# Kernel tuning notes

Measured on AMD Instinct MI355X. Metric: run time of the kernel, lower is better.

The kernel has to match this reference:

```python
import jax, jax.numpy as jnp
import numpy as np

VOCAB = 512
T = 64
D = 32
N_NODES = 4000
N_LAYERS = 5
EDGE_P = 0.03
N_BIAS = 2
SEED = 0
BATCH = 512
N_IN = T * D  # 2048 input nodes (flattened [T, d_model])


def build_graph():
    """Deterministic layered random-wired DAG.

    Node layout: [0, N_IN) inputs | [N_IN, N_IN+N_BIAS) bias(=1) |
    hidden layers | last VOCAB nodes = outputs (logits).
    An edge (u -> v) exists with prob EDGE_P for any u in an earlier
    layer than v; every non-input node gets >=1 incoming edge.
    Returns (layers, total_edges) where each layer entry is
    (src_ids, dst_local, layer_start, layer_size, w_lo, w_hi).
    """
    rng = np.random.RandomState(SEED)
    n_hidden = N_NODES - (N_IN + N_BIAS) - VOCAB
    sizes = [n_hidden // N_LAYERS + (1 if i < n_hidden % N_LAYERS else 0)
             for i in range(N_LAYERS)] + [VOCAB]
    layers = []
    start = N_IN + N_BIAS  # nodes with ids < start are valid sources
    offset = 0
    for size in sizes:
        mask = rng.random((start, size)) < EDGE_P
        empty = np.where(mask.sum(axis=0) == 0)[0]
        if empty.size:
            mask[rng.randint(0, start, empty.size), empty] = True
        src, dst = np.nonzero(mask)
        n_e = src.size
        layers.append((src.astype(np.int32), dst.astype(np.int32),
                       start, size, offset, offset + n_e))
        offset += n_e
        start += size
    return layers, offset


def setup_inputs() -> dict:
    key = jax.random.key(0)
    k1, k2, k3, k4 = jax.random.split(key, 4)
    _, n_edges = build_graph()
    return {
        "ids": jax.random.randint(k1, (BATCH, T), 0, VOCAB),
        "token_emb": jax.random.normal(k2, (VOCAB, D), dtype=jnp.float32) * 0.02,
        "pos_emb": jax.random.normal(k3, (T, D), dtype=jnp.float32) * 0.02,
        "weights": jax.random.normal(k4, (n_edges,), dtype=jnp.float32) * 0.05,
    }


def reference(ids, token_emb, pos_emb, weights):
    layers, _ = build_graph()  # static (numpy, trace-time)
    B = ids.shape[0]
    # embedding lookup + positional add, flatten to the RWNN input slab
    emb = token_emb[ids] + pos_emb[None, :, :]          # [B, T, D]
    flat = emb.reshape(B, N_IN)                          # [B, n_in]
    vals = jnp.concatenate(
        [flat, jnp.ones((B, N_BIAS), flat.dtype)], axis=1)  # [B, n_in+n_bias]
    n_layers_total = len(layers)
    for li, (src, dst, start, size, w0, w1) in enumerate(layers):
        # irregular gather over all predecessor nodes, scale, scatter-add
        msg = vals[:, src] * weights[w0:w1]              # [B, E_l]
        pre = jnp.zeros((B, size), flat.dtype).at[:, dst].add(msg)
        h = pre if li == n_layers_total - 1 else jnp.tanh(pre)
        vals = jnp.concatenate([vals, h], axis=1)
    return vals[:, -VOCAB:]                              # logits [B, V]
```

## Files before the change

### kernel.cpp

```cpp
#include <hip/hip_runtime.h>
#include <cstdint>
#include <cstdlib>
#include <cstring>
#include <vector>

#define RW_VOCAB 512
#define RW_T 64
#define RW_NIN 2048
#define RW_NBIAS 2
#define RW_BATCH 512
#define RW_NLAYERS 6
#define RW_VBLD 4096

typedef __attribute__((ext_vector_type(8))) short short8;
typedef __attribute__((ext_vector_type(4))) float f32x4;
typedef uint32_t u32;

namespace {

struct MT19937 {
  uint32_t mt[624];
  int mti;
  void seed(uint32_t s) {
    for (int i = 0; i < 624; ++i) {
      mt[i] = s;
      s = 1812433253u * (s ^ (s >> 30)) + (uint32_t)i + 1u;
    }
    mti = 624;
  }
  inline uint32_t next() {
    if (mti >= 624) {
      for (int i = 0; i < 624; ++i) {
        uint32_t y = (mt[i] & 0x80000000u) | (mt[(i + 1) % 624] & 0x7fffffffu);
        mt[i] = mt[(i + 397) % 624] ^ (y >> 1) ^ ((y & 1u) ? 2567483615u : 0u);
      }
      mti = 0;
    }
    uint32_t y = mt[mti++];
    y ^= y >> 11;
    y ^= (y << 7) & 2636928640u;
    y ^= (y << 15) & 4022730752u;
    y ^= y >> 18;
    return y;
  }
  inline double rnd() {
    uint32_t a = next() >> 5, b = next() >> 6;
    return ((double)a * 67108864.0 + (double)b) / 9007199254740992.0;
  }
};

const int LAYER_SIZES[RW_NLAYERS] = {288, 288, 288, 287, 287, 512};
const int LAYER_START[RW_NLAYERS] = {2050, 2338, 2626, 2914, 3201, 3488};
const int LAYER_NPAD[RW_NLAYERS] = {288, 288, 288, 288, 288, 512};
const int LAYER_NT[RW_NLAYERS] = {9, 9, 9, 9, 9, 16};
const int LAYER_SK[RW_NLAYERS] = {7, 7, 7, 7, 7, 4};

struct GArgsH {
  int p0[RW_NLAYERS], ep[RW_NLAYERS], er[RW_NLAYERS], w0[RW_NLAYERS];
  int kpad[RW_NLAYERS];
  unsigned wofs[RW_NLAYERS];
};

struct HostGraph {
  int Epad;
  GArgsH ga;
  unsigned wdt_elems;
  uint32_t* h_pack;
};

HostGraph* build_host_graph() {
  auto* G = new HostGraph();
  MT19937 mt;
  mt.seed(0);
  std::vector<uint32_t> pack;
  pack.reserve(180000);
  int start = RW_NIN + RW_NBIAS;
  int wcum = 0;
  for (int li = 0; li < RW_NLAYERS; ++li) {
    const int size = LAYER_SIZES[li];
    G->ga.p0[li] = (int)pack.size();
    G->ga.w0[li] = wcum;
    int cnt = 0;
    for (int u = 0; u < start; ++u) {
      for (int v = 0; v < size; ++v) {
        if (mt.rnd() < 0.03) {
          pack.push_back(((uint32_t)v << 12) | (uint32_t)u);
          ++cnt;
        }
      }
    }
    G->ga.er[li] = cnt;
    wcum += cnt;
    while (pack.size() & 3u) pack.push_back(0u);
    G->ga.ep[li] = (int)pack.size() - G->ga.p0[li];
    start += size;
  }
  G->Epad = (int)pack.size();
  unsigned ofs = 0;
  for (int li = 0; li < RW_NLAYERS; ++li) {
    G->ga.kpad[li] = ((LAYER_START[li] + 63) / 64) * 64;
    G->ga.wofs[li] = ofs;
    ofs += (unsigned)LAYER_NPAD[li] * (unsigned)G->ga.kpad[li];
  }
  G->wdt_elems = ofs;
  const size_t bytes = (size_t)G->Epad * 4;
  if (hipHostMalloc((void**)&G->h_pack, bytes) != hipSuccess)
    G->h_pack = (uint32_t*)malloc(bytes);
  memcpy(G->h_pack, pack.data(), bytes);
  return G;
}

}

struct GArgs {
  int p0[RW_NLAYERS], ep[RW_NLAYERS], er[RW_NLAYERS], w0[RW_NLAYERS];
  int kpad[RW_NLAYERS];
  unsigned wofs[RW_NLAYERS];
};

__device__ __forceinline__ unsigned short f2bf(float f) {
  unsigned u = __builtin_bit_cast(unsigned, f);
  return (unsigned short)((u + 0x7fffu + ((u >> 16) & 1u)) >> 16);
}

__global__ __launch_bounds__(256) void rwnn_init(
    uint4* __restrict__ wdt4, int n4, uint4* __restrict__ pre4,
    uint4* __restrict__ vb4, const int* __restrict__ ids,
    const float* __restrict__ tok, const float* __restrict__ pos) {
  const int gt = blockIdx.x * 256 + threadIdx.x;
  const int gs = gridDim.x * 256;
  const uint4 z = {0u, 0u, 0u, 0u};
  for (int i = gt; i < n4; i += gs) wdt4[i] = z;
  for (int i = gt; i < RW_BATCH * 512 / 4; i += gs) pre4[i] = z;
  for (int i = gt; i < RW_BATCH * (RW_VBLD / 8); i += gs) {
    const int b = i >> 9, j = i & 511;
    const int c0 = j * 8;
    uint4 val = z;
    if (c0 + 8 <= RW_NIN) {
      const int id = ids[b * RW_T + (c0 >> 5)];
      const float4 t0 = *(const float4*)(tok + id * 32 + (c0 & 31));
      const float4 t1 = *(const float4*)(tok + id * 32 + (c0 & 31) + 4);
      const float4 p0 = *(const float4*)(pos + c0);
      const float4 p1 = *(const float4*)(pos + c0 + 4);
      val.x = (u32)f2bf(t0.x + p0.x) | ((u32)f2bf(t0.y + p0.y) << 16);
      val.y = (u32)f2bf(t0.z + p0.z) | ((u32)f2bf(t0.w + p0.w) << 16);
      val.z = (u32)f2bf(t1.x + p1.x) | ((u32)f2bf(t1.y + p1.y) << 16);
      val.w = (u32)f2bf(t1.z + p1.z) | ((u32)f2bf(t1.w + p1.w) << 16);
    } else if (c0 == RW_NIN) {
      val.x = 0x3f803f80u;
    }
    vb4[(size_t)b * (RW_VBLD / 8) + j] = val;
  }
}

__global__ __launch_bounds__(256) void rwnn_scatter(
    const uint32_t* __restrict__ pack, const float* __restrict__ w,
    unsigned short* __restrict__ wdt, GArgs ga, int Epad) {
  const int i = blockIdx.x * 256 + threadIdx.x;
  if (i >= Epad) return;
  int l = 0;
#pragma unroll
  for (int k = 1; k < RW_NLAYERS; ++k)
    if (i >= ga.p0[k]) l = k;
  const int kk = i - ga.p0[l];
  if (kk >= ga.er[l]) return;
  const uint32_t pk = pack[i];
  const unsigned u = pk & 4095u, v = pk >> 12;
  wdt[ga.wofs[l] + (size_t)v * (unsigned)ga.kpad[l] + u] =
      f2bf(w[ga.w0[l] + kk]);
}

__global__ __launch_bounds__(256) void rwnn_gemm(
    const unsigned short* __restrict__ Vb,
    const unsigned short* __restrict__ Bt, float* __restrict__ pre, int kpad,
    int ck) {
  __shared__ unsigned short As[128 * 64];
  __shared__ unsigned short Bs[32 * 64];
  const int tid = threadIdx.x;
  const int wave = tid >> 6, lane = tid & 63;
  const int mt = blockIdx.x, nt = blockIdx.y, sk = blockIdx.z;
  const int k0 = sk * ck;
  const int k1 = min(k0 + ck, kpad);
  const int nit = (k1 - k0 + 63) >> 6;

  const int arow = tid >> 3;
  const int ach = tid & 7;
  const int aswz = (ach ^ (arow & 7)) << 4;
  const unsigned short* gA =
      Vb + (size_t)(mt * 128 + arow) * RW_VBLD + ach * 8;
  const unsigned short* gB = Bt + (size_t)(nt * 32 + arow) * kpad + ach * 8;
  float4 pfa0, pfa1, pfa2, pfa3, pfb;

#define LOADREGS(kk)                                                      \
  do {                                                                    \
    pfa0 = *(const float4*)(gA + (kk));                                   \
    pfa1 = *(const float4*)(gA + (size_t)32 * RW_VBLD + (kk));            \
    pfa2 = *(const float4*)(gA + (size_t)64 * RW_VBLD + (kk));            \
    pfa3 = *(const float4*)(gA + (size_t)96 * RW_VBLD + (kk));            \
    pfb = *(const float4*)(gB + (kk));                                    \
  } while (0)

  LOADREGS(k0);

  const int lr = lane & 15, gc4 = lane >> 4;
  f32x4 acc[2][2] = {};

  for (int t = 0; t < nit; ++t) {
    __syncthreads();
    *(float4*)((char*)As + (arow)*128 + aswz) = pfa0;
    *(float4*)((char*)As + (32 + arow) * 128 + aswz) = pfa1;
    *(float4*)((char*)As + (64 + arow) * 128 + aswz) = pfa2;
    *(float4*)((char*)As + (96 + arow) * 128 + aswz) = pfa3;
    *(float4*)((char*)Bs + arow * 128 + aswz) = pfb;
    __syncthreads();
    if (t + 1 < nit) LOADREGS(k0 + (t + 1) * 64);
#pragma unroll
    for (int kk = 0; kk < 2; ++kk) {
      const int sa = ((kk * 4 + gc4) ^ (lr & 7)) << 4;
      const short8 a0 =
          *(const short8*)((char*)As + (wave * 32 + lr) * 128 + sa);
      const short8 a1 =
          *(const short8*)((char*)As + (wave * 32 + 16 + lr) * 128 + sa);
      const short8 b0 = *(const short8*)((char*)Bs + lr * 128 + sa);
      const short8 b1 = *(const short8*)((char*)Bs + (16 + lr) * 128 + sa);
      acc[0][0] =
          __builtin_amdgcn_mfma_f32_16x16x32_bf16(a0, b0, acc[0][0], 0, 0, 0);
      acc[0][1] =
          __builtin_amdgcn_mfma_f32_16x16x32_bf16(a0, b1, acc[0][1], 0, 0, 0);
      acc[1][0] =
          __builtin_amdgcn_mfma_f32_16x16x32_bf16(a1, b0, acc[1][0], 0, 0, 0);
      acc[1][1] =
          __builtin_amdgcn_mfma_f32_16x16x32_bf16(a1, b1, acc[1][1], 0, 0, 0);
    }
  }
#undef LOADREGS

  const int lq = lane >> 4;
#pragma unroll
  for (int ms = 0; ms < 2; ++ms)
#pragma unroll
    for (int ns = 0; ns < 2; ++ns)
#pragma unroll
      for (int r = 0; r < 4; ++r) {
        const int grow = mt * 128 + wave * 32 + ms * 16 + lq * 4 + r;
        const int gcol = nt * 32 + ns * 16 + lr;
        atomicAdd(pre + (size_t)grow * 512 + gcol, acc[ms][ns][r]);
      }
}

__global__ __launch_bounds__(256) void rwnn_epi(
    float* __restrict__ pre, unsigned short* __restrict__ Vb,
    float* __restrict__ out, int start, int nsize, int last) {
  const int b = blockIdx.x;
  for (int n = threadIdx.x; n < 512; n += 256) {
    const float v = pre[(size_t)b * 512 + n];
    pre[(size_t)b * 512 + n] = 0.0f;
    if (n < nsize) {
      if (last)
        out[(size_t)b * 512 + n] = v;
      else
        Vb[(size_t)b * RW_VBLD + start + n] = f2bf(tanhf(v));
    }
  }
}

__global__ __launch_bounds__(256) void rwnn_build_w(const float* __restrict__ w,
                                                    float* __restrict__ wpad,
                                                    GArgs ga, int Epad) {
  const int i = blockIdx.x * 256 + threadIdx.x;
  if (i >= Epad) return;
  int l = 0;
#pragma unroll
  for (int k = 1; k < RW_NLAYERS; ++k)
    if (i >= ga.p0[k]) l = k;
  const int kk = i - ga.p0[l];
  wpad[i] = (kk < ga.er[l]) ? w[ga.w0[l] + kk] : 0.0f;
}

__global__ __launch_bounds__(512) void rwnn_fwd_sparse(
    const int* __restrict__ ids, const float* __restrict__ tok,
    const float* __restrict__ pos, const uint32_t* __restrict__ pack,
    const float* __restrict__ wpad, float* __restrict__ out, GArgs ga) {
  __shared__ float vals[4000];
  const int b = blockIdx.x;
  const int tid = threadIdx.x;
  for (int i = tid; i < RW_NIN; i += 512) {
    const int t = i >> 5, d = i & 31;
    vals[i] = tok[(ids[b * RW_T + t] << 5) + d] + pos[i];
  }
  if (tid < RW_NBIAS) vals[RW_NIN + tid] = 1.0f;
  const int sizes[RW_NLAYERS] = {288, 288, 288, 287, 287, 512};
  int nb = RW_NIN + RW_NBIAS;
  for (int li = 0; li < RW_NLAYERS; ++li) {
    const int size = sizes[li];
    __syncthreads();
    for (int v = tid; v < size; v += 512) vals[nb + v] = 0.0f;
    __syncthreads();
    const int p0 = ga.p0[li], ng = ga.ep[li] >> 2;
    for (int g = tid; g < ng; g += 512) {
      const int e = p0 + (g << 2);
      const uint4 pk = *reinterpret_cast<const uint4*>(pack + e);
      const float4 wv = *reinterpret_cast<const float4*>(wpad + e);
      atomicAdd(&vals[nb + (pk.x >> 12)], vals[pk.x & 4095u] * wv.x);
      atomicAdd(&vals[nb + (pk.y >> 12)], vals[pk.y & 4095u] * wv.y);
      atomicAdd(&vals[nb + (pk.z >> 12)], vals[pk.z & 4095u] * wv.z);
      atomicAdd(&vals[nb + (pk.w >> 12)], vals[pk.w & 4095u] * wv.w);
    }
    __syncthreads();
    if (li == RW_NLAYERS - 1) {
      for (int v = tid; v < RW_VOCAB; v += 512)
        out[b * RW_VOCAB + v] = vals[nb + v];
    } else {
      for (int v = tid; v < size; v += 512) vals[nb + v] = tanhf(vals[nb + v]);
    }
    nb += size;
  }
}

extern "C" void kernel_launch(void* const* d_in, const int* in_sizes, int n_in,
                              void* d_out, int out_size, void* d_ws,
                              size_t ws_size, hipStream_t stream) {
  static HostGraph* G = build_host_graph();
  const int Epad = G->Epad;

  const int* ids = (const int*)d_in[0];
  const float* tok = (const float*)d_in[1];
  const float* pos = (const float*)d_in[2];
  const float* w = (const float*)d_in[3];
  float* out = (float*)d_out;

  GArgs ga;
  memcpy(&ga, &G->ga, sizeof(GArgs));

  char* ws = (char*)d_ws;
  const size_t packB = ((size_t)Epad * 4 + 255) & ~(size_t)255;
  const size_t wdtB = ((size_t)G->wdt_elems * 2 + 255) & ~(size_t)255;
  const size_t vbB = (size_t)RW_BATCH * RW_VBLD * 2;
  const size_t preB = (size_t)RW_BATCH * 512 * 4;
  const size_t need = packB + wdtB + vbB + preB;

  uint32_t* d_pack = (uint32_t*)ws;
  hipMemcpyAsync(d_pack, G->h_pack, (size_t)Epad * 4, hipMemcpyHostToDevice,
                 stream);

  if (ws_size < need) {
    float* d_wpad = (float*)(ws + packB);
    rwnn_build_w<<<(Epad + 255) / 256, 256, 0, stream>>>(w, d_wpad, ga, Epad);
    rwnn_fwd_sparse<<<RW_BATCH, 512, 0, stream>>>(ids, tok, pos, d_pack,
                                                  d_wpad, out, ga);
    return;
  }

  unsigned short* d_wdt = (unsigned short*)(ws + packB);
  unsigned short* d_vb = (unsigned short*)(ws + packB + wdtB);
  float* d_pre = (float*)(ws + packB + wdtB + vbB);

  rwnn_init<<<1024, 256, 0, stream>>>((uint4*)d_wdt, (int)(G->wdt_elems / 8),
                                      (uint4*)d_pre, (uint4*)d_vb, ids, tok,
                                      pos);
  rwnn_scatter<<<(Epad + 255) / 256, 256, 0, stream>>>(d_pack, w, d_wdt, ga,
                                                       Epad);
  for (int l = 0; l < RW_NLAYERS; ++l) {
    const int SK = LAYER_SK[l];
    const int kpad = ga.kpad[l];
    const int ck = ((kpad + SK - 1) / SK + 63) & ~63;
    rwnn_gemm<<<dim3(4, LAYER_NT[l], SK), 256, 0, stream>>>(
        d_vb, d_wdt + ga.wofs[l], d_pre, kpad, ck);
    rwnn_epi<<<RW_BATCH, 256, 0, stream>>>(d_pre, d_vb, out, LAYER_START[l],
                                           LAYER_SIZES[l],
                                           l == RW_NLAYERS - 1 ? 1 : 0);
  }
}
```

Measured before the change: 155.8 us.

## Fuse init, scatter, per-layer GEMMs and epilogues into one cooperative kernel

Replaces the chain of init, scatter, and per-layer GEMM plus epilogue launches (14 kernels) with a single persistent cooperative kernel of 256 blocks. Stages are separated by grid-wide syncs, and each block's work for a layer is found from its block index. This removes per-launch overhead and the pipeline drains between small kernels. In exchange, every stage is capped at 256 blocks, the epilogue now handles two rows per block, and each grid.sync has its own cost.

New measurement: 518.4 us. 233% more time.

```diff
diff --git a/kernel.cpp b/kernel.cpp
--- a/kernel.cpp
+++ b/kernel.cpp
@@ -1,8 +1,11 @@
 #include <hip/hip_runtime.h>
+#include <hip/hip_cooperative_groups.h>
 #include <cstdint>
 #include <cstdlib>
 #include <cstring>
 #include <vector>
+
+namespace cg = cooperative_groups;
 
 #define RW_VOCAB 512
 #define RW_T 64
@@ -11,6 +14,7 @@
 #define RW_BATCH 512
 #define RW_NLAYERS 6
 #define RW_VBLD 4096
+#define NBLK 256
 
 typedef __attribute__((ext_vector_type(8))) short short8;
 typedef __attribute__((ext_vector_type(4))) float f32x4;
@@ -55,15 +59,16 @@
 const int LAYER_NT[RW_NLAYERS] = {9, 9, 9, 9, 9, 16};
 const int LAYER_SK[RW_NLAYERS] = {7, 7, 7, 7, 7, 4};
 
-struct GArgsH {
+struct FArgsH {
   int p0[RW_NLAYERS], ep[RW_NLAYERS], er[RW_NLAYERS], w0[RW_NLAYERS];
-  int kpad[RW_NLAYERS];
+  int kpad[RW_NLAYERS], ck[RW_NLAYERS], sk[RW_NLAYERS], nt[RW_NLAYERS];
+  int nsize[RW_NLAYERS], vstart[RW_NLAYERS];
   unsigned wofs[RW_NLAYERS];
+  int Epad, nwdt4;
 };
 
 struct HostGraph {
-  int Epad;
-  GArgsH ga;
+  FArgsH fa;
   unsigned wdt_elems;
   uint32_t* h_pack;
 };
@@ -78,8 +83,8 @@
   int wcum = 0;
   for (int li = 0; li < RW_NLAYERS; ++li) {
     const int size = LAYER_SIZES[li];
-    G->ga.p0[li] = (int)pack.size();
-    G->ga.w0[li] = wcum;
+    G->fa.p0[li] = (int)pack.size();
+    G->fa.w0[li] = wcum;
     int cnt = 0;
     for (int u = 0; u < start; ++u) {
       for (int v = 0; v < size; ++v) {
@@ -89,21 +94,28 @@
         }
       }
     }
-    G->ga.er[li] = cnt;
+    G->fa.er[li] = cnt;
     wcum += cnt;
     while (pack.size() & 3u) pack.push_back(0u);
-    G->ga.ep[li] = (int)pack.size() - G->ga.p0[li];
+    G->fa.ep[li] = (int)pack.size() - G->fa.p0[li];
     start += size;
   }
-  G->Epad = (int)pack.size();
+  G->fa.Epad = (int)pack.size();
   unsigned ofs = 0;
   for (int li = 0; li < RW_NLAYERS; ++li) {
-    G->ga.kpad[li] = ((LAYER_START[li] + 63) / 64) * 64;
-    G->ga.wofs[li] = ofs;
-    ofs += (unsigned)LAYER_NPAD[li] * (unsigned)G->ga.kpad[li];
+    G->fa.kpad[li] = ((LAYER_START[li] + 63) / 64) * 64;
+    G->fa.wofs[li] = ofs;
+    ofs += (unsigned)LAYER_NPAD[li] * (unsigned)G->fa.kpad[li];
+    G->fa.sk[li] = LAYER_SK[li];
+    G->fa.nt[li] = LAYER_NT[li];
+    G->fa.nsize[li] = LAYER_SIZES[li];
+    G->fa.vstart[li] = LAYER_START[li];
+    G->fa.ck[li] = ((G->fa.kpad[li] + LAYER_SK[li] - 1) / LAYER_SK[li] + 63) &
+                   ~63;
   }
   G->wdt_elems = ofs;
-  const size_t bytes = (size_t)G->Epad * 4;
+  G->fa.nwdt4 = (int)(ofs / 8);
+  const size_t bytes = (size_t)G->fa.Epad * 4;
   if (hipHostMalloc((void**)&G->h_pack, bytes) != hipSuccess)
     G->h_pack = (uint32_t*)malloc(bytes);
   memcpy(G->h_pack, pack.data(), bytes);
@@ -112,10 +124,12 @@
 
 }
 
-struct GArgs {
+struct FArgs {
   int p0[RW_NLAYERS], ep[RW_NLAYERS], er[RW_NLAYERS], w0[RW_NLAYERS];
-  int kpad[RW_NLAYERS];
+  int kpad[RW_NLAYERS], ck[RW_NLAYERS], sk[RW_NLAYERS], nt[RW_NLAYERS];
+  int nsize[RW_NLAYERS], vstart[RW_NLAYERS];
   unsigned wofs[RW_NLAYERS];
+  int Epad, nwdt4;
 };
 
 __device__ __forceinline__ unsigned short f2bf(float f) {
@@ -123,150 +137,170 @@
   return (unsigned short)((u + 0x7fffu + ((u >> 16) & 1u)) >> 16);
 }
 
-__global__ __launch_bounds__(256) void rwnn_init(
-    uint4* __restrict__ wdt4, int n4, uint4* __restrict__ pre4,
-    uint4* __restrict__ vb4, const int* __restrict__ ids,
-    const float* __restrict__ tok, const float* __restrict__ pos) {
-  const int gt = blockIdx.x * 256 + threadIdx.x;
-  const int gs = gridDim.x * 256;
-  const uint4 z = {0u, 0u, 0u, 0u};
-  for (int i = gt; i < n4; i += gs) wdt4[i] = z;
-  for (int i = gt; i < RW_BATCH * 512 / 4; i += gs) pre4[i] = z;
-  for (int i = gt; i < RW_BATCH * (RW_VBLD / 8); i += gs) {
-    const int b = i >> 9, j = i & 511;
-    const int c0 = j * 8;
-    uint4 val = z;
-    if (c0 + 8 <= RW_NIN) {
-      const int id = ids[b * RW_T + (c0 >> 5)];
-      const float4 t0 = *(const float4*)(tok + id * 32 + (c0 & 31));
-      const float4 t1 = *(const float4*)(tok + id * 32 + (c0 & 31) + 4);
-      const float4 p0 = *(const float4*)(pos + c0);
-      const float4 p1 = *(const float4*)(pos + c0 + 4);
-      val.x = (u32)f2bf(t0.x + p0.x) | ((u32)f2bf(t0.y + p0.y) << 16);
-      val.y = (u32)f2bf(t0.z + p0.z) | ((u32)f2bf(t0.w + p0.w) << 16);
-      val.z = (u32)f2bf(t1.x + p1.x) | ((u32)f2bf(t1.y + p1.y) << 16);
-      val.w = (u32)f2bf(t1.z + p1.z) | ((u32)f2bf(t1.w + p1.w) << 16);
-    } else if (c0 == RW_NIN) {
-      val.x = 0x3f803f80u;
-    }
-    vb4[(size_t)b * (RW_VBLD / 8) + j] = val;
-  }
-}
-
-__global__ __launch_bounds__(256) void rwnn_scatter(
+__global__ __launch_bounds__(256) void rwnn_fused(
     const uint32_t* __restrict__ pack, const float* __restrict__ w,
-    unsigned short* __restrict__ wdt, GArgs ga, int Epad) {
-  const int i = blockIdx.x * 256 + threadIdx.x;
-  if (i >= Epad) return;
-  int l = 0;
-#pragma unroll
-  for (int k = 1; k < RW_NLAYERS; ++k)
-    if (i >= ga.p0[k]) l = k;
-  const int kk = i - ga.p0[l];
-  if (kk >= ga.er[l]) return;
-  const uint32_t pk = pack[i];
-  const unsigned u = pk & 4095u, v = pk >> 12;
-  wdt[ga.wofs[l] + (size_t)v * (unsigned)ga.kpad[l] + u] =
-      f2bf(w[ga.w0[l] + kk]);
-}
-
-__global__ __launch_bounds__(256) void rwnn_gemm(
-    const unsigned short* __restrict__ Vb,
-    const unsigned short* __restrict__ Bt, float* __restrict__ pre, int kpad,
-    int ck) {
+    unsigned short* __restrict__ wdt, unsigned short* __restrict__ vb,
+    float* __restrict__ pre, const int* __restrict__ ids,
+    const float* __restrict__ tok, const float* __restrict__ pos,
+    float* __restrict__ out, FArgs ga) {
+  cg::grid_group grid = cg::this_grid();
   __shared__ unsigned short As[128 * 64];
   __shared__ unsigned short Bs[32 * 64];
   const int tid = threadIdx.x;
+  const int bid = blockIdx.x;
+  const int gt = bid * 256 + tid;
+  const int gs = NBLK * 256;
+
+  {
+    const uint4 z = {0u, 0u, 0u, 0u};
+    uint4* wdt4 = (uint4*)wdt;
+    for (int i = gt; i < ga.nwdt4; i += gs) wdt4[i] = z;
+    uint4* pre4 = (uint4*)pre;
+    for (int i = gt; i < RW_BATCH * 512 / 4; i += gs) pre4[i] = z;
+    uint4* vb4 = (uint4*)vb;
+    for (int i = gt; i < RW_BATCH * (RW_VBLD / 8); i += gs) {
+      const int b = i >> 9, j = i & 511;
+      const int c0 = j * 8;
+      uint4 val = z;
+      if (c0 + 8 <= RW_NIN) {
+        const int id = ids[b * RW_T + (c0 >> 5)];
+        const float4 t0 = *(const float4*)(tok + id * 32 + (c0 & 31));
+        const float4 t1 = *(const float4*)(tok + id * 32 + (c0 & 31) + 4);
+        const float4 p0 = *(const float4*)(pos + c0);
+        const float4 p1 = *(const float4*)(pos + c0 + 4);
+        val.x = (u32)f2bf(t0.x + p0.x) | ((u32)f2bf(t0.y + p0.y) << 16);
+        val.y = (u32)f2bf(t0.z + p0.z) | ((u32)f2bf(t0.w + p0.w) << 16);
+        val.z = (u32)f2bf(t1.x + p1.x) | ((u32)f2bf(t1.y + p1.y) << 16);
+        val.w = (u32)f2bf(t1.z + p1.z) | ((u32)f2bf(t1.w + p1.w) << 16);
+      } else if (c0 == RW_NIN) {
+        val.x = 0x3f803f80u;
+      }
+      vb4[(size_t)b * (RW_VBLD / 8) + j] = val;
+    }
+  }
+  grid.sync();
+
+  for (int i = gt; i < ga.Epad; i += gs) {
+    int l = 0;
+#pragma unroll
+    for (int k = 1; k < RW_NLAYERS; ++k)
+      if (i >= ga.p0[k]) l = k;
+    const int kk = i - ga.p0[l];
+    if (kk < ga.er[l]) {
+      const uint32_t pk = pack[i];
+      const unsigned u = pk & 4095u, v = pk >> 12;
+      wdt[ga.wofs[l] + (size_t)v * (unsigned)ga.kpad[l] + u] =
+          f2bf(w[ga.w0[l] + kk]);
+    }
+  }
+  grid.sync();
+
   const int wave = tid >> 6, lane = tid & 63;
-  const int mt = blockIdx.x, nt = blockIdx.y, sk = blockIdx.z;
-  const int k0 = sk * ck;
-  const int k1 = min(k0 + ck, kpad);
-  const int nit = (k1 - k0 + 63) >> 6;
-
+  const int lr = lane & 15, gc4 = lane >> 4, lq = lane >> 4;
   const int arow = tid >> 3;
   const int ach = tid & 7;
   const int aswz = (ach ^ (arow & 7)) << 4;
-  const unsigned short* gA =
-      Vb + (size_t)(mt * 128 + arow) * RW_VBLD + ach * 8;
-  const unsigned short* gB = Bt + (size_t)(nt * 32 + arow) * kpad + ach * 8;
-  float4 pfa0, pfa1, pfa2, pfa3, pfb;
-
-#define LOADREGS(kk)                                                      \
-  do {                                                                    \
-    pfa0 = *(const float4*)(gA + (kk));                                   \
-    pfa1 = *(const float4*)(gA + (size_t)32 * RW_VBLD + (kk));            \
-    pfa2 = *(const float4*)(gA + (size_t)64 * RW_VBLD + (kk));            \
-    pfa3 = *(const float4*)(gA + (size_t)96 * RW_VBLD + (kk));            \
-    pfb = *(const float4*)(gB + (kk));                                    \
+
+  for (int l = 0; l < RW_NLAYERS; ++l) {
+    const int SK = ga.sk[l], NT = ga.nt[l];
+    const int kpad = ga.kpad[l], ck = ga.ck[l];
+    const int mt = bid & 3;
+    const int rest = bid >> 2;
+    const int nt_ = rest % NT;
+    const int sk_ = rest / NT;
+
+    if (sk_ < SK) {
+      const unsigned short* Bt = wdt + ga.wofs[l];
+      const int k0 = sk_ * ck;
+      const int k1 = min(k0 + ck, kpad);
+      const int nit = (k1 - k0 + 63) >> 6;
+
+      const unsigned short* gA =
+          vb + (size_t)(mt * 128 + arow) * RW_VBLD + ach * 8;
+      const unsigned short* gB =
+          Bt + (size_t)(nt_ * 32 + arow) * kpad + ach * 8;
+      float4 pfa0, pfa1, pfa2, pfa3, pfb;
+
+#define LOADREGS(kk)                                                  \
+  do {                                                                \
+    pfa0 = *(const float4*)(gA + (kk));                               \
+    pfa1 = *(const float4*)(gA + (size_t)32 * RW_VBLD + (kk));        \
+    pfa2 = *(const float4*)(gA + (size_t)64 * RW_VBLD + (kk));        \
+    pfa3 = *(const float4*)(gA + (size_t)96 * RW_VBLD + (kk));        \
+    pfb = *(const float4*)(gB + (kk));                                \
   } while (0)
 
-  LOADREGS(k0);
-
-  const int lr = lane & 15, gc4 = lane >> 4;
-  f32x4 acc[2][2] = {};
-
-  for (int t = 0; t < nit; ++t) {
-    __syncthreads();
-    *(float4*)((char*)As + (arow)*128 + aswz) = pfa0;
-    *(float4*)((char*)As + (32 + arow) * 128 + aswz) = pfa1;
-    *(float4*)((char*)As + (64 + arow) * 128 + aswz) = pfa2;
-    *(float4*)((char*)As + (96 + arow) * 128 + aswz) = pfa3;
-    *(float4*)((char*)Bs + arow * 128 + aswz) = pfb;
-    __syncthreads();
-    if (t + 1 < nit) LOADREGS(k0 + (t + 1) * 64);
-#pragma unroll
-    for (int kk = 0; kk < 2; ++kk) {
-      const int sa = ((kk * 4 + gc4) ^ (lr & 7)) << 4;
-      const short8 a0 =
-          *(const short8*)((char*)As + (wave * 32 + lr) * 128 + sa);
-      const short8 a1 =
-          *(const short8*)((char*)As + (wave * 32 + 16 + lr) * 128 + sa);
-      const short8 b0 = *(const short8*)((char*)Bs + lr * 128 + sa);
-      const short8 b1 = *(const short8*)((char*)Bs + (16 + lr) * 128 + sa);
-      acc[0][0] =
-          __builtin_amdgcn_mfma_f32_16x16x32_bf16(a0, b0, acc[0][0], 0, 0, 0);
-      acc[0][1] =
-          __builtin_amdgcn_mfma_f32_16x16x32_bf16(a0, b1, acc[0][1], 0, 0, 0);
-      acc[1][0] =
-          __builtin_amdgcn_mfma_f32_16x16x32_bf16(a1, b0, acc[1][0], 0, 0, 0);
-      acc[1][1] =
-          __builtin_amdgcn_mfma_f32_16x16x32_bf16(a1, b1, acc[1][1], 0, 0, 0);
-    }
-  }
+      LOADREGS(k0);
+      f32x4 acc[2][2] = {};
+
+      for (int t = 0; t < nit; ++t) {
+        __syncthreads();
+        *(float4*)((char*)As + (arow)*128 + aswz) = pfa0;
+        *(float4*)((char*)As + (32 + arow) * 128 + aswz) = pfa1;
+        *(float4*)((char*)As + (64 + arow) * 128 + aswz) = pfa2;
+        *(float4*)((char*)As + (96 + arow) * 128 + aswz) = pfa3;
+        *(float4*)((char*)Bs + arow * 128 + aswz) = pfb;
+        __syncthreads();
+        if (t + 1 < nit) LOADREGS(k0 + (t + 1) * 64);
+#pragma unroll
+        for (int kk = 0; kk < 2; ++kk) {
+          const int sa = ((kk * 4 + gc4) ^ (lr & 7)) << 4;
+          const short8 a0 =
+              *(const short8*)((char*)As + (wave * 32 + lr) * 128 + sa);
+          const short8 a1 =
+              *(const short8*)((char*)As + (wave * 32 + 16 + lr) * 128 + sa);
+          const short8 b0 = *(const short8*)((char*)Bs + lr * 128 + sa);
+          const short8 b1 = *(const short8*)((char*)Bs + (16 + lr) * 128 + sa);
+          acc[0][0] = __builtin_amdgcn_mfma_f32_16x16x32_bf16(a0, b0,
+                                                              acc[0][0], 0, 0, 0);
+          acc[0][1] = __builtin_amdgcn_mfma_f32_16x16x32_bf16(a0, b1,
+                                                              acc[0][1], 0, 0, 0);
+          acc[1][0] = __builtin_amdgcn_mfma_f32_16x16x32_bf16(a1, b0,
+                                                              acc[1][0], 0, 0, 0);
+          acc[1][1] = __builtin_amdgcn_mfma_f32_16x16x32_bf16(a1, b1,
+                                                              acc[1][1], 0, 0, 0);
+        }
+      }
 #undef LOADREGS
 
-  const int lq = lane >> 4;
-#pragma unroll
-  for (int ms = 0; ms < 2; ++ms)
-#pragma unroll
-    for (int ns = 0; ns < 2; ++ns)
-#pragma unroll
-      for (int r = 0; r < 4; ++r) {
-        const int grow = mt * 128 + wave * 32 + ms * 16 + lq * 4 + r;
-        const int gcol = nt * 32 + ns * 16 + lr;
-        atomicAdd(pre + (size_t)grow * 512 + gcol, acc[ms][ns][r]);
-      }
-}
-
-__global__ __launch_bounds__(256) void rwnn_epi(
-    float* __restrict__ pre, unsigned short* __restrict__ Vb,
-    float* __restrict__ out, int start, int nsize, int last) {
-  const int b = blockIdx.x;
-  for (int n = threadIdx.x; n < 512; n += 256) {
-    const float v = pre[(size_t)b * 512 + n];
-    pre[(size_t)b * 512 + n] = 0.0f;
-    if (n < nsize) {
-      if (last)
-        out[(size_t)b * 512 + n] = v;
-      else
-        Vb[(size_t)b * RW_VBLD + start + n] = f2bf(tanhf(v));
-    }
+#pragma unroll
+      for (int ms = 0; ms < 2; ++ms)
+#pragma unroll
+        for (int ns = 0; ns < 2; ++ns)
+#pragma unroll
+          for (int r = 0; r < 4; ++r) {
+            const int grow = mt * 128 + wave * 32 + ms * 16 + lq * 4 + r;
+            const int gcol = nt_ * 32 + ns * 16 + lr;
+            atomicAdd(pre + (size_t)grow * 512 + gcol, acc[ms][ns][r]);
+          }
+    }
+    grid.sync();
+
+    {
+      const int nsize = ga.nsize[l], vstart = ga.vstart[l];
+      const int last = (l == RW_NLAYERS - 1);
+#pragma unroll
+      for (int rr = 0; rr < 2; ++rr) {
+        const int b = bid * 2 + rr;
+        for (int n = tid; n < 512; n += 256) {
+          const float v = pre[(size_t)b * 512 + n];
+          pre[(size_t)b * 512 + n] = 0.0f;
+          if (n < nsize) {
+            if (last)
+              out[(size_t)b * 512 + n] = v;
+            else
+              vb[(size_t)b * RW_VBLD + vstart + n] = f2bf(tanhf(v));
+          }
+        }
+      }
+    }
+    if (l + 1 < RW_NLAYERS) grid.sync();
   }
 }
 
 __global__ __launch_bounds__(256) void rwnn_build_w(const float* __restrict__ w,
                                                     float* __restrict__ wpad,
-                                                    GArgs ga, int Epad) {
+                                                    FArgs ga, int Epad) {
   const int i = blockIdx.x * 256 + threadIdx.x;
   if (i >= Epad) return;
   int l = 0;
@@ -280,7 +314,7 @@
 __global__ __launch_bounds__(512) void rwnn_fwd_sparse(
     const int* __restrict__ ids, const float* __restrict__ tok,
     const float* __restrict__ pos, const uint32_t* __restrict__ pack,
-    const float* __restrict__ wpad, float* __restrict__ out, GArgs ga) {
+    const float* __restrict__ wpad, float* __restrict__ out, FArgs ga) {
   __shared__ float vals[4000];
   const int b = blockIdx.x;
   const int tid = threadIdx.x;
@@ -321,7 +355,7 @@
                               void* d_out, int out_size, void* d_ws,
                               size_t ws_size, hipStream_t stream) {
   static HostGraph* G = build_host_graph();
-  const int Epad = G->Epad;
+  const int Epad = G->fa.Epad;
 
   const int* ids = (const int*)d_in[0];
   const float* tok = (const float*)d_in[1];
@@ -329,8 +363,8 @@
   const float* w = (const float*)d_in[3];
   float* out = (float*)d_out;
 
-  GArgs ga;
-  memcpy(&ga, &G->ga, sizeof(GArgs));
+  FArgs ga;
+  memcpy(&ga, &G->fa, sizeof(FArgs));
 
   char* ws = (char*)d_ws;
   const size_t packB = ((size_t)Epad * 4 + 255) & ~(size_t)255;
@@ -355,19 +389,9 @@
   unsigned short* d_vb = (unsigned short*)(ws + packB + wdtB);
   float* d_pre = (float*)(ws + packB + wdtB + vbB);
 
-  rwnn_init<<<1024, 256, 0, stream>>>((uint4*)d_wdt, (int)(G->wdt_elems / 8),
-                                      (uint4*)d_pre, (uint4*)d_vb, ids, tok,
-                                      pos);
-  rwnn_scatter<<<(Epad + 255) / 256, 256, 0, stream>>>(d_pack, w, d_wdt, ga,
-                                                       Epad);
-  for (int l = 0; l < RW_NLAYERS; ++l) {
-    const int SK = LAYER_SK[l];
-    const int kpad = ga.kpad[l];
-    const int ck = ((kpad + SK - 1) / SK + 63) & ~63;
-    rwnn_gemm<<<dim3(4, LAYER_NT[l], SK), 256, 0, stream>>>(
-        d_vb, d_wdt + ga.wofs[l], d_pre, kpad, ck);
-    rwnn_epi<<<RW_BATCH, 256, 0, stream>>>(d_pre, d_vb, out, LAYER_START[l],
-                                           LAYER_SIZES[l],
-                                           l == RW_NLAYERS - 1 ? 1 : 0);
-  }
-}
+  void* kargs[] = {(void*)&d_pack, (void*)&w,   (void*)&d_wdt,
+                   (void*)&d_vb,   (void*)&d_pre, (void*)&ids,
+                   (void*)&tok,    (void*)&pos, (void*)&out, (void*)&ga};
+  hipLaunchCooperativeKernel((const void*)rwnn_fused, dim3(NBLK), dim3(256),
+                             kargs, 0, stream);
+}
```
